# Performance work log

Hardware: AMD Instinct MI355X
Metric: run time of the kernel (lower is better)

The kernel has to match this reference:

```python
import jax, jax.numpy as jnp
import numpy as np

D_MODEL = 1024
N_HEADS = 16
D_K = D_MODEL // N_HEADS
THETA = 10000.0
BATCH = 2
SEQ = 2048


def apply_rope(x, positions):
    # x: [B, H, S, d_k], positions: [S] int
    half = D_K // 2
    inv_freq = 1.0 / (THETA ** (jnp.arange(half, dtype=jnp.float32) * 2.0 / D_K))  # [half]
    ang = positions.astype(jnp.float32)[:, None] * inv_freq[None, :]  # [S, half]
    cos = jnp.cos(ang)
    sin = jnp.sin(ang)
    xr = x.reshape(x.shape[:-1] + (half, 2))
    x1, x2 = xr[..., 0], xr[..., 1]
    o1 = x1 * cos - x2 * sin
    o2 = x1 * sin + x2 * cos
    return jnp.stack([o1, o2], axis=-1).reshape(x.shape)


def setup_inputs() -> dict:
    key = jax.random.key(0)
    ks = jax.random.split(key, 5)
    scale = 1.0 / np.sqrt(D_MODEL)
    return {
        "x": jax.random.normal(ks[0], (BATCH, SEQ, D_MODEL), jnp.float32),
        "token_positions": jnp.arange(SEQ, dtype=jnp.int32),
        "Wq": jax.random.normal(ks[1], (D_MODEL, D_MODEL), jnp.float32) * scale,
        "Wk": jax.random.normal(ks[2], (D_MODEL, D_MODEL), jnp.float32) * scale,
        "Wv": jax.random.normal(ks[3], (D_MODEL, D_MODEL), jnp.float32) * scale,
        "Wo": jax.random.normal(ks[4], (D_MODEL, D_MODEL), jnp.float32) * scale,
    }


def reference(x, token_positions, Wq, Wk, Wv, Wo):
    B, S, _ = x.shape
    # projections (Linear with weight [out, in], no bias): y = x @ W^T
    def split_heads(t):
        return t.reshape(B, S, N_HEADS, D_K).transpose(0, 2, 1, 3)  # [B,H,S,d_k]

    Q = split_heads(x @ Wq.T)
    K = split_heads(x @ Wk.T)
    V = split_heads(x @ Wv.T)

    Q = apply_rope(Q, token_positions)
    K = apply_rope(K, token_positions)

    scores = jnp.einsum("bhqd,bhkd->bhqk", Q, K) / np.sqrt(D_K)
    causal = jnp.tril(jnp.ones((S, S), dtype=bool))
    scores = jnp.where(causal, scores, -jnp.inf)
    attn = jax.nn.softmax(scores, axis=-1)
    out = jnp.einsum("bhqk,bhkd->bhqd", attn, V)  # [B,H,S,d_k]
    out = out.transpose(0, 2, 1, 3).reshape(B, S, D_MODEL)
    return out @ Wo.T
```

## Files before the change

### kernel.cpp

```cpp
#include <hip/hip_runtime.h>
#include <hip/hip_bf16.h>


typedef __bf16 bf16x8 __attribute__((ext_vector_type(8)));
typedef __bf16 bf16x4 __attribute__((ext_vector_type(4)));
typedef float f32x4 __attribute__((ext_vector_type(4)));
typedef unsigned short ushort8 __attribute__((ext_vector_type(8)));

#define BATCH 2
#define SEQ 2048
#define NH 16
#define DK 64
#define DM 1024
#define BH (BATCH*NH)
#define M_TOT (BATCH*SEQ)

__device__ __forceinline__ void gload16(const void* g, void* l) {
    __builtin_amdgcn_global_load_lds((const __attribute__((address_space(1))) void*)g,
                                     (__attribute__((address_space(3))) void*)l, 16, 0, 0);
}

__global__ void cvt_kernel(const float* __restrict__ s, __bf16* __restrict__ d, int n) {
    int i = (blockIdx.x * blockDim.x + threadIdx.x) * 4;
    if (i >= n) return;
    float4 v = *(const float4*)(s + i);
    bf16x4 o;
    o[0] = (__bf16)v.x; o[1] = (__bf16)v.y; o[2] = (__bf16)v.z; o[3] = (__bf16)v.w;
    *(bf16x4*)(d + i) = o;
}

__global__ void cvt4_kernel(const float* __restrict__ s0, const float* __restrict__ s1,
                            const float* __restrict__ s2, const float* __restrict__ s3,
                            __bf16* __restrict__ d0, __bf16* __restrict__ d1,
                            __bf16* __restrict__ d2, __bf16* __restrict__ d3, int n) {
    const int z = blockIdx.y;
    const float* s = (z == 0) ? s0 : (z == 1) ? s1 : (z == 2) ? s2 : s3;
    __bf16* d = (z == 0) ? d0 : (z == 1) ? d1 : (z == 2) ? d2 : d3;
    int i = (blockIdx.x * blockDim.x + threadIdx.x) * 4;
    if (i >= n) return;
    float4 v = *(const float4*)(s + i);
    bf16x4 o;
    o[0] = (__bf16)v.x; o[1] = (__bf16)v.y; o[2] = (__bf16)v.z; o[3] = (__bf16)v.w;
    *(bf16x4*)(d + i) = o;
}

__device__ __forceinline__ void gemm_tile_compute(
    const __bf16* __restrict__ A, const __bf16* __restrict__ W,
    int m0, int n0, int K, __bf16* sA, __bf16* sB, f32x4 (&acc)[4][4])
{
    const int t = threadIdx.x;
    const int lane = t & 63, wid = t >> 6;
    const int wr = wid >> 1, wc = wid & 1;
    const int g = lane >> 4, l15 = lane & 15;

    f32x4 zero = {0.f, 0.f, 0.f, 0.f};
#pragma unroll
    for (int mt = 0; mt < 4; ++mt)
#pragma unroll
        for (int nt = 0; nt < 4; ++nt) acc[mt][nt] = zero;

    for (int k0 = 0; k0 < K; k0 += 32) {
        __syncthreads();
#pragma unroll
        for (int rnd = 0; rnd < 2; ++rnd) {
            int s = rnd * 256 + t;
            int row = s >> 2, ch = s & 3;
            __bf16* dstA = sA + (rnd * 256 + wid * 64) * 8;
            __bf16* dstB = sB + (rnd * 256 + wid * 64) * 8;
            gload16(A + (size_t)(m0 + row) * K + k0 + ch * 8, dstA);
            gload16(W + (size_t)(n0 + row) * K + k0 + ch * 8, dstB);
        }
        __syncthreads();
        bf16x8 af[4], bfr[4];
#pragma unroll
        for (int mt = 0; mt < 4; ++mt)
            af[mt] = *(const bf16x8*)&sA[(wr * 64 + mt * 16 + l15) * 32 + g * 8];
#pragma unroll
        for (int nt = 0; nt < 4; ++nt)
            bfr[nt] = *(const bf16x8*)&sB[(wc * 64 + nt * 16 + l15) * 32 + g * 8];
#pragma unroll
        for (int mt = 0; mt < 4; ++mt)
#pragma unroll
            for (int nt = 0; nt < 4; ++nt)
                acc[mt][nt] = __builtin_amdgcn_mfma_f32_16x16x32_bf16(af[mt], bfr[nt], acc[mt][nt], 0, 0, 0);
    }
}

__global__ __launch_bounds__(256) void gemm_qkv(
    const __bf16* __restrict__ xb, const __bf16* __restrict__ wqkv,
    __bf16* __restrict__ Qb, __bf16* __restrict__ Kb, __bf16* __restrict__ VTb)
{
    __shared__ __align__(16) __bf16 sA[128 * 32], sB[128 * 32];
    int id = blockIdx.x + 24 * blockIdx.y;
    id = (id & 7) * 96 + (id >> 3);
    const int m0 = (id / 24) * 128, n0 = (id % 24) * 128;

    f32x4 acc[4][4];
    gemm_tile_compute(xb, wqkv, m0, n0, DM, sA, sB, acc);

    const int t = threadIdx.x, lane = t & 63, wid = t >> 6;
    const int wr = wid >> 1, wc = wid & 1, g = lane >> 4, l15 = lane & 15;
#pragma unroll
    for (int mt = 0; mt < 4; ++mt)
#pragma unroll
        for (int nt = 0; nt < 4; ++nt)
#pragma unroll
            for (int r = 0; r < 4; ++r) {
                int m = m0 + wr * 64 + mt * 16 + g * 4 + r;
                int n = n0 + wc * 64 + nt * 16 + l15;
                int z = n >> 10, hd = n & 1023, h = hd >> 6, d = hd & 63;
                int b = m >> 11, s = m & 2047;
                __bf16 v = (__bf16)acc[mt][nt][r];
                if (z == 0)
                    Qb[(((size_t)(b * NH + h)) * SEQ + s) * DK + d] = v;
                else if (z == 1)
                    Kb[(((size_t)(b * NH + h)) * SEQ + s) * DK + d] = v;
                else
                    VTb[(((size_t)(b * NH + h)) * DK + d) * SEQ + s] = v;
            }
}

__global__ __launch_bounds__(256) void gemm_out(
    const __bf16* __restrict__ AO, const __bf16* __restrict__ wo, float* __restrict__ out)
{
    __shared__ __align__(16) __bf16 sA[128 * 32], sB[128 * 32];
    int id = blockIdx.x + 8 * blockIdx.y;
    id = (id & 7) * 32 + (id >> 3);
    const int m0 = (id / 8) * 128, n0 = (id % 8) * 128;

    f32x4 acc[4][4];
    gemm_tile_compute(AO, wo, m0, n0, DM, sA, sB, acc);

    const int t = threadIdx.x, lane = t & 63, wid = t >> 6;
    const int wr = wid >> 1, wc = wid & 1, g = lane >> 4, l15 = lane & 15;
#pragma unroll
    for (int mt = 0; mt < 4; ++mt)
#pragma unroll
        for (int nt = 0; nt < 4; ++nt)
#pragma unroll
            for (int r = 0; r < 4; ++r) {
                int m = m0 + wr * 64 + mt * 16 + g * 4 + r;
                int n = n0 + wc * 64 + nt * 16 + l15;
                out[(size_t)m * DM + n] = acc[mt][nt][r];
            }
}

__global__ __launch_bounds__(256) void rope_kernel(
    __bf16* __restrict__ Qb, __bf16* __restrict__ Kb, const int* __restrict__ pos)
{
    __shared__ float ctab[32], stab[32];
    const int s = blockIdx.x;
    const int t = threadIdx.x;
    if (t < 32) {
        float invf = exp2f(-13.287712379549449f * (float)t * (1.0f / 32.0f));
        float ang = (float)pos[s] * invf;
        float sn, cs;
        sincosf(ang, &sn, &cs);
        ctab[t] = cs; stab[t] = sn;
    }
    __syncthreads();
#pragma unroll
    for (int u = 0; u < 8; ++u) {
        int id = u * 256 + t;
        int i = id & 31;
        int bh = (id >> 5) & 31;
        int isK = id >> 10;
        __bf16* P = isK ? Kb : Qb;
        float qs = isK ? 1.0f : 0.125f;
        __bf16* p = P + ((size_t)bh * SEQ + s) * DK + i * 2;
        float x1 = (float)p[0], x2 = (float)p[1];
        float c = ctab[i], sn = stab[i];
        p[0] = (__bf16)(qs * (x1 * c - x2 * sn));
        p[1] = (__bf16)(qs * (x1 * sn + x2 * c));
    }
}

__global__ __launch_bounds__(256, 2) void attn_kernel(
    const __bf16* __restrict__ Qb, const __bf16* __restrict__ Kb,
    const __bf16* __restrict__ VTb, __bf16* __restrict__ AO)
{
    __shared__ __align__(16) __bf16 sK[2][64 * 64];
    __shared__ __align__(16) __bf16 sV[2][64 * 64];
    __shared__ __align__(16) __bf16 sP[4 * 16 * 64];

    const int n = blockIdx.x;
    const int xcd = n & 7, slot = n >> 3;
    const int bh = xcd * 4 + (slot >> 4);
    const int x = slot & 15;
    const int t = threadIdx.x, lane = t & 63, wid = t >> 6;
    const int g = lane >> 4, l15 = lane & 15;

    const size_t baseQK = (size_t)bh * SEQ * DK;
    const size_t baseVT = (size_t)bh * DK * SEQ;
    const int b = bh >> 4, h = bh & 15;

    const char* Kt0 = (const char*)(Kb + baseQK);
    const char* Vt0 = (const char*)(VTb + baseVT);
    char* myP = (char*)sP + wid * 2048;
    f32x4 zero = {0.f, 0.f, 0.f, 0.f};

    auto stage_tile = [&](int kt, int bq) {
        const char* Kt = Kt0 + (size_t)kt * 64 * 128;
        const char* Vt = Vt0 + (size_t)kt * 128;
#pragma unroll
        for (int cc = 0; cc < 2; ++cc) {
            int c = t + cc * 256;
            int r = c >> 3, pp = c & 7;
            int p = pp ^ (r & 7);
            char* bK = (char*)sK[bq] + (cc * 256 + wid * 64) * 16;
            char* bV = (char*)sV[bq] + (cc * 256 + wid * 64) * 16;
            gload16(Kt + (size_t)r * 128 + p * 16, bK);
            gload16(Vt + (size_t)r * (SEQ * 2) + p * 16, bV);
        }
    };

    for (int ph = 0; ph < 2; ++ph) {
        const int j = ph ? (31 - x) : x;
        const int qrow_w = j * 64 + wid * 16;
        const int ktmax = j;

        bf16x8 qf[2];
        {
            const __bf16* qp = Qb + baseQK + (size_t)(qrow_w + l15) * DK;
            qf[0] = *(const bf16x8*)(qp + g * 8);
            qf[1] = *(const bf16x8*)(qp + 32 + g * 8);
        }

        f32x4 oacc[4];
        float mrow[4], lacc[4];
#pragma unroll
        for (int dt = 0; dt < 4; ++dt) oacc[dt] = zero;
#pragma unroll
        for (int r = 0; r < 4; ++r) { mrow[r] = -3e38f; lacc[r] = 0.f; }

        stage_tile(0, 0);
        __syncthreads();
        int cur = 0;

        for (int kt = 0; kt <= ktmax; ++kt) {
            if (kt < ktmax) stage_tile(kt + 1, cur ^ 1);

            f32x4 sacc[4];
#pragma unroll
            for (int nt = 0; nt < 4; ++nt) {
                sacc[nt] = zero;
                int row = nt * 16 + l15;
#pragma unroll
                for (int ks = 0; ks < 2; ++ks) {
                    bf16x8 kf = *(const bf16x8*)((const char*)sK[cur] + row * 128 +
                                                 ((ks * 64 + g * 16) ^ ((row & 7) << 4)));
                    sacc[nt] = __builtin_amdgcn_mfma_f32_16x16x32_bf16(qf[ks], kf, sacc[nt], 0, 0, 0);
                }
            }

            if (kt == ktmax) {
#pragma unroll
                for (int nt = 0; nt < 4; ++nt)
#pragma unroll
                    for (int r = 0; r < 4; ++r) {
                        int kv = kt * 64 + nt * 16 + l15;
                        int q = qrow_w + g * 4 + r;
                        if (kv > q) sacc[nt][r] = -3e38f;
                    }
            }

#pragma unroll
            for (int r = 0; r < 4; ++r) {
                float tm = fmaxf(fmaxf(sacc[0][r], sacc[1][r]), fmaxf(sacc[2][r], sacc[3][r]));
#pragma unroll
                for (int msk = 1; msk < 16; msk <<= 1) tm = fmaxf(tm, __shfl_xor(tm, msk));
                if (tm > mrow[r] + 8.0f) {
                    float sc = __expf(mrow[r] - tm);
                    mrow[r] = tm;
                    lacc[r] *= sc;
#pragma unroll
                    for (int dt = 0; dt < 4; ++dt) oacc[dt][r] *= sc;
                }
#pragma unroll
                for (int nt = 0; nt < 4; ++nt) {
                    float p = __expf(sacc[nt][r] - mrow[r]);
                    sacc[nt][r] = p;
                    lacc[r] += p;
                }
            }

#pragma unroll
            for (int nt = 0; nt < 4; ++nt)
#pragma unroll
                for (int r = 0; r < 4; ++r) {
                    int row = g * 4 + r;
                    *(__bf16*)(myP + row * 128 +
                               ((nt * 32 + l15 * 2) ^ ((row & 7) << 4))) = (__bf16)sacc[nt][r];
                }

#pragma unroll
            for (int ks = 0; ks < 2; ++ks) {
                bf16x8 pf = *(const bf16x8*)(myP + l15 * 128 +
                                             ((ks * 64 + g * 16) ^ ((l15 & 7) << 4)));
#pragma unroll
                for (int dt = 0; dt < 4; ++dt) {
                    int row = dt * 16 + l15;
                    bf16x8 vf = *(const bf16x8*)((const char*)sV[cur] + row * 128 +
                                                 ((ks * 64 + g * 16) ^ ((row & 7) << 4)));
                    oacc[dt] = __builtin_amdgcn_mfma_f32_16x16x32_bf16(pf, vf, oacc[dt], 0, 0, 0);
                }
            }

            __syncthreads();
            cur ^= 1;
        }

#pragma unroll
        for (int r = 0; r < 4; ++r) {
            float rs = lacc[r];
#pragma unroll
            for (int msk = 1; msk < 16; msk <<= 1) rs += __shfl_xor(rs, msk);
            float inv = 1.0f / rs;
            int srow = qrow_w + g * 4 + r;
            size_t obase = ((size_t)b * SEQ + srow) * DM + h * DK;
#pragma unroll
            for (int dt = 0; dt < 4; ++dt)
                AO[obase + dt * 16 + l15] = (__bf16)(oacc[dt][r] * inv);
        }
    }
}

extern "C" void kernel_launch(void* const* d_in, const int* in_sizes, int n_in,
                              void* d_out, int out_size, void* d_ws, size_t ws_size,
                              hipStream_t stream) {
    (void)in_sizes; (void)n_in; (void)out_size; (void)ws_size;
    const float* x  = (const float*)d_in[0];
    const int*  pos = (const int*)d_in[1];
    const float* Wq = (const float*)d_in[2];
    const float* Wk = (const float*)d_in[3];
    const float* Wv = (const float*)d_in[4];
    const float* Wo = (const float*)d_in[5];
    float* out = (float*)d_out;

    char* ws = (char*)d_ws;
    __bf16* xb   = (__bf16*)ws; ws += (size_t)M_TOT * DM * 2;
    __bf16* wqkv = (__bf16*)ws; ws += (size_t)3 * DM * DM * 2;
    __bf16* wob  = (__bf16*)ws; ws += (size_t)DM * DM * 2;
    __bf16* Qb   = (__bf16*)ws; ws += (size_t)BH * SEQ * DK * 2;
    __bf16* Kb   = (__bf16*)ws; ws += (size_t)BH * SEQ * DK * 2;
    __bf16* VTb  = (__bf16*)ws; ws += (size_t)BH * SEQ * DK * 2;
    __bf16* AOb  = (__bf16*)ws; ws += (size_t)M_TOT * DM * 2;

    const int nx = M_TOT * DM, nw = DM * DM;
    cvt_kernel<<<nx / 4 / 256, 256, 0, stream>>>(x, xb, nx);
    cvt4_kernel<<<dim3(nw / 4 / 256, 4), 256, 0, stream>>>(
        Wq, Wk, Wv, Wo, wqkv, wqkv + nw, wqkv + 2 * nw, wob, nw);

    gemm_qkv<<<dim3(24, M_TOT / 128), 256, 0, stream>>>(xb, wqkv, Qb, Kb, VTb);
    rope_kernel<<<SEQ, 256, 0, stream>>>(Qb, Kb, pos);
    attn_kernel<<<512, 256, 0, stream>>>(Qb, Kb, VTb, AOb);
    gemm_out<<<dim3(8, M_TOT / 128), 256, 0, stream>>>(AOb, wob, out);
}
```

Baseline: 220.3 us.

## Merge convert kernels, split attention into one query tile per block, use exp2

The two fp32-to-bf16 conversion kernels become a single launch. Attention blocks now each handle one 64-row query tile instead of a paired short/long tile, which doubles the grid to 1024 blocks and interleaves long and short tiles across blocks. Q is pre-scaled by log2(e) so the softmax can use exp2f, and MFMA sections are wrapped with s_setprio. Both GEMMs gain a launch_bounds occupancy hint. The risk is that per-block causal work becomes unbalanced, since pairing tiles no longer evens out the load inside a block.

```diff
diff --git a/kernel.cpp b/kernel.cpp
--- a/kernel.cpp
+++ b/kernel.cpp
@@ -14,34 +14,35 @@
 #define DM 1024
 #define BH (BATCH*NH)
 #define M_TOT (BATCH*SEQ)
+#define NX (M_TOT*DM)
+#define NW (DM*DM)
 
 __device__ __forceinline__ void gload16(const void* g, void* l) {
     __builtin_amdgcn_global_load_lds((const __attribute__((address_space(1))) void*)g,
                                      (__attribute__((address_space(3))) void*)l, 16, 0, 0);
 }
 
-__global__ void cvt_kernel(const float* __restrict__ s, __bf16* __restrict__ d, int n) {
-    int i = (blockIdx.x * blockDim.x + threadIdx.x) * 4;
-    if (i >= n) return;
-    float4 v = *(const float4*)(s + i);
+__global__ void cvt_all(const float* __restrict__ x,
+                        const float* __restrict__ Wq, const float* __restrict__ Wk,
+                        const float* __restrict__ Wv, const float* __restrict__ Wo,
+                        __bf16* __restrict__ xb, __bf16* __restrict__ wqkv,
+                        __bf16* __restrict__ wob) {
+    int i4 = (blockIdx.x * blockDim.x + threadIdx.x) * 4;
+    const float* s;
+    __bf16* d;
+    int off;
+    if (i4 < NX) { s = x; d = xb; off = i4; }
+    else {
+        int j = i4 - NX;
+        int z = j >> 20;
+        off = j & (NW - 1);
+        s = (z == 0) ? Wq : (z == 1) ? Wk : (z == 2) ? Wv : Wo;
+        d = (z == 3) ? wob : wqkv + (size_t)z * NW;
+    }
+    float4 v = *(const float4*)(s + off);
     bf16x4 o;
     o[0] = (__bf16)v.x; o[1] = (__bf16)v.y; o[2] = (__bf16)v.z; o[3] = (__bf16)v.w;
-    *(bf16x4*)(d + i) = o;
-}
-
-__global__ void cvt4_kernel(const float* __restrict__ s0, const float* __restrict__ s1,
-                            const float* __restrict__ s2, const float* __restrict__ s3,
-                            __bf16* __restrict__ d0, __bf16* __restrict__ d1,
-                            __bf16* __restrict__ d2, __bf16* __restrict__ d3, int n) {
-    const int z = blockIdx.y;
-    const float* s = (z == 0) ? s0 : (z == 1) ? s1 : (z == 2) ? s2 : s3;
-    __bf16* d = (z == 0) ? d0 : (z == 1) ? d1 : (z == 2) ? d2 : d3;
-    int i = (blockIdx.x * blockDim.x + threadIdx.x) * 4;
-    if (i >= n) return;
-    float4 v = *(const float4*)(s + i);
-    bf16x4 o;
-    o[0] = (__bf16)v.x; o[1] = (__bf16)v.y; o[2] = (__bf16)v.z; o[3] = (__bf16)v.w;
-    *(bf16x4*)(d + i) = o;
+    *(bf16x4*)(d + off) = o;
 }
 
 __device__ __forceinline__ void gemm_tile_compute(
@@ -86,7 +87,7 @@
     }
 }
 
-__global__ __launch_bounds__(256) void gemm_qkv(
+__global__ __launch_bounds__(256, 2) void gemm_qkv(
     const __bf16* __restrict__ xb, const __bf16* __restrict__ wqkv,
     __bf16* __restrict__ Qb, __bf16* __restrict__ Kb, __bf16* __restrict__ VTb)
 {
@@ -120,7 +121,7 @@
             }
 }
 
-__global__ __launch_bounds__(256) void gemm_out(
+__global__ __launch_bounds__(256, 2) void gemm_out(
     const __bf16* __restrict__ AO, const __bf16* __restrict__ wo, float* __restrict__ out)
 {
     __shared__ __align__(16) __bf16 sA[128 * 32], sB[128 * 32];
@@ -166,7 +167,7 @@
         int bh = (id >> 5) & 31;
         int isK = id >> 10;
         __bf16* P = isK ? Kb : Qb;
-        float qs = isK ? 1.0f : 0.125f;
+        float qs = isK ? 1.0f : (0.125f * 1.44269504088896f);
         __bf16* p = P + ((size_t)bh * SEQ + s) * DK + i * 2;
         float x1 = (float)p[0], x2 = (float)p[1];
         float c = ctab[i], sn = stab[i];
@@ -185,14 +186,17 @@
 
     const int n = blockIdx.x;
     const int xcd = n & 7, slot = n >> 3;
-    const int bh = xcd * 4 + (slot >> 4);
-    const int x = slot & 15;
+    const int bh = xcd * 4 + (slot >> 5);
+    const int js = slot & 31;
+    const int j = (js & 1) ? (js >> 1) : (31 - (js >> 1));
     const int t = threadIdx.x, lane = t & 63, wid = t >> 6;
     const int g = lane >> 4, l15 = lane & 15;
 
     const size_t baseQK = (size_t)bh * SEQ * DK;
     const size_t baseVT = (size_t)bh * DK * SEQ;
     const int b = bh >> 4, h = bh & 15;
+    const int qrow_w = j * 64 + wid * 16;
+    const int ktmax = j;
 
     const char* Kt0 = (const char*)(Kb + baseQK);
     const char* Vt0 = (const char*)(VTb + baseVT);
@@ -214,114 +218,113 @@
         }
     };
 
-    for (int ph = 0; ph < 2; ++ph) {
-        const int j = ph ? (31 - x) : x;
-        const int qrow_w = j * 64 + wid * 16;
-        const int ktmax = j;
-
-        bf16x8 qf[2];
-        {
-            const __bf16* qp = Qb + baseQK + (size_t)(qrow_w + l15) * DK;
-            qf[0] = *(const bf16x8*)(qp + g * 8);
-            qf[1] = *(const bf16x8*)(qp + 32 + g * 8);
-        }
-
-        f32x4 oacc[4];
-        float mrow[4], lacc[4];
-#pragma unroll
-        for (int dt = 0; dt < 4; ++dt) oacc[dt] = zero;
-#pragma unroll
-        for (int r = 0; r < 4; ++r) { mrow[r] = -3e38f; lacc[r] = 0.f; }
-
-        stage_tile(0, 0);
+    stage_tile(0, 0);
+
+    bf16x8 qf[2];
+    {
+        const __bf16* qp = Qb + baseQK + (size_t)(qrow_w + l15) * DK;
+        qf[0] = *(const bf16x8*)(qp + g * 8);
+        qf[1] = *(const bf16x8*)(qp + 32 + g * 8);
+    }
+
+    f32x4 oacc[4];
+    float mrow[4], lacc[4];
+#pragma unroll
+    for (int dt = 0; dt < 4; ++dt) oacc[dt] = zero;
+#pragma unroll
+    for (int r = 0; r < 4; ++r) { mrow[r] = -3e38f; lacc[r] = 0.f; }
+
+    __syncthreads();
+    int cur = 0;
+
+    for (int kt = 0; kt <= ktmax; ++kt) {
+        if (kt < ktmax) stage_tile(kt + 1, cur ^ 1);
+
+        f32x4 sacc[4];
+        __builtin_amdgcn_s_setprio(1);
+#pragma unroll
+        for (int nt = 0; nt < 4; ++nt) {
+            sacc[nt] = zero;
+            int row = nt * 16 + l15;
+#pragma unroll
+            for (int ks = 0; ks < 2; ++ks) {
+                bf16x8 kf = *(const bf16x8*)((const char*)sK[cur] + row * 128 +
+                                             ((ks * 64 + g * 16) ^ ((row & 7) << 4)));
+                sacc[nt] = __builtin_amdgcn_mfma_f32_16x16x32_bf16(qf[ks], kf, sacc[nt], 0, 0, 0);
+            }
+        }
+        __builtin_amdgcn_s_setprio(0);
+
+        if (kt == ktmax) {
+#pragma unroll
+            for (int nt = 0; nt < 4; ++nt)
+#pragma unroll
+                for (int r = 0; r < 4; ++r) {
+                    int kv = kt * 64 + nt * 16 + l15;
+                    int q = qrow_w + g * 4 + r;
+                    if (kv > q) sacc[nt][r] = -3e38f;
+                }
+        }
+
+#pragma unroll
+        for (int r = 0; r < 4; ++r) {
+            float tm = fmaxf(fmaxf(sacc[0][r], sacc[1][r]), fmaxf(sacc[2][r], sacc[3][r]));
+#pragma unroll
+            for (int msk = 1; msk < 16; msk <<= 1) tm = fmaxf(tm, __shfl_xor(tm, msk));
+            if (tm > mrow[r] + 11.5416f) {
+                float sc = exp2f(mrow[r] - tm);
+                mrow[r] = tm;
+                lacc[r] *= sc;
+#pragma unroll
+                for (int dt = 0; dt < 4; ++dt) oacc[dt][r] *= sc;
+            }
+#pragma unroll
+            for (int nt = 0; nt < 4; ++nt) {
+                float p = exp2f(sacc[nt][r] - mrow[r]);
+                sacc[nt][r] = p;
+                lacc[r] += p;
+            }
+        }
+
+#pragma unroll
+        for (int nt = 0; nt < 4; ++nt)
+#pragma unroll
+            for (int r = 0; r < 4; ++r) {
+                int row = g * 4 + r;
+                *(__bf16*)(myP + row * 128 +
+                           ((nt * 32 + l15 * 2) ^ ((row & 7) << 4))) = (__bf16)sacc[nt][r];
+            }
+
+        __builtin_amdgcn_s_setprio(1);
+#pragma unroll
+        for (int ks = 0; ks < 2; ++ks) {
+            bf16x8 pf = *(const bf16x8*)(myP + l15 * 128 +
+                                         ((ks * 64 + g * 16) ^ ((l15 & 7) << 4)));
+#pragma unroll
+            for (int dt = 0; dt < 4; ++dt) {
+                int row = dt * 16 + l15;
+                bf16x8 vf = *(const bf16x8*)((const char*)sV[cur] + row * 128 +
+                                             ((ks * 64 + g * 16) ^ ((row & 7) << 4)));
+                oacc[dt] = __builtin_amdgcn_mfma_f32_16x16x32_bf16(pf, vf, oacc[dt], 0, 0, 0);
+            }
+        }
+        __builtin_amdgcn_s_setprio(0);
+
         __syncthreads();
-        int cur = 0;
-
-        for (int kt = 0; kt <= ktmax; ++kt) {
-            if (kt < ktmax) stage_tile(kt + 1, cur ^ 1);
-
-            f32x4 sacc[4];
-#pragma unroll
-            for (int nt = 0; nt < 4; ++nt) {
-                sacc[nt] = zero;
-                int row = nt * 16 + l15;
-#pragma unroll
-                for (int ks = 0; ks < 2; ++ks) {
-                    bf16x8 kf = *(const bf16x8*)((const char*)sK[cur] + row * 128 +
-                                                 ((ks * 64 + g * 16) ^ ((row & 7) << 4)));
-                    sacc[nt] = __builtin_amdgcn_mfma_f32_16x16x32_bf16(qf[ks], kf, sacc[nt], 0, 0, 0);
-                }
-            }
-
-            if (kt == ktmax) {
-#pragma unroll
-                for (int nt = 0; nt < 4; ++nt)
-#pragma unroll
-                    for (int r = 0; r < 4; ++r) {
-                        int kv = kt * 64 + nt * 16 + l15;
-                        int q = qrow_w + g * 4 + r;
-                        if (kv > q) sacc[nt][r] = -3e38f;
-                    }
-            }
-
-#pragma unroll
-            for (int r = 0; r < 4; ++r) {
-                float tm = fmaxf(fmaxf(sacc[0][r], sacc[1][r]), fmaxf(sacc[2][r], sacc[3][r]));
-#pragma unroll
-                for (int msk = 1; msk < 16; msk <<= 1) tm = fmaxf(tm, __shfl_xor(tm, msk));
-                if (tm > mrow[r] + 8.0f) {
-                    float sc = __expf(mrow[r] - tm);
-                    mrow[r] = tm;
-                    lacc[r] *= sc;
-#pragma unroll
-                    for (int dt = 0; dt < 4; ++dt) oacc[dt][r] *= sc;
-                }
-#pragma unroll
-                for (int nt = 0; nt < 4; ++nt) {
-                    float p = __expf(sacc[nt][r] - mrow[r]);
-                    sacc[nt][r] = p;
-                    lacc[r] += p;
-                }
-            }
-
-#pragma unroll
-            for (int nt = 0; nt < 4; ++nt)
-#pragma unroll
-                for (int r = 0; r < 4; ++r) {
-                    int row = g * 4 + r;
-                    *(__bf16*)(myP + row * 128 +
-                               ((nt * 32 + l15 * 2) ^ ((row & 7) << 4))) = (__bf16)sacc[nt][r];
-                }
-
-#pragma unroll
-            for (int ks = 0; ks < 2; ++ks) {
-                bf16x8 pf = *(const bf16x8*)(myP + l15 * 128 +
-                                             ((ks * 64 + g * 16) ^ ((l15 & 7) << 4)));
-#pragma unroll
-                for (int dt = 0; dt < 4; ++dt) {
-                    int row = dt * 16 + l15;
-                    bf16x8 vf = *(const bf16x8*)((const char*)sV[cur] + row * 128 +
-                                                 ((ks * 64 + g * 16) ^ ((row & 7) << 4)));
-                    oacc[dt] = __builtin_amdgcn_mfma_f32_16x16x32_bf16(pf, vf, oacc[dt], 0, 0, 0);
-                }
-            }
-
-            __syncthreads();
-            cur ^= 1;
-        }
-
-#pragma unroll
-        for (int r = 0; r < 4; ++r) {
-            float rs = lacc[r];
-#pragma unroll
-            for (int msk = 1; msk < 16; msk <<= 1) rs += __shfl_xor(rs, msk);
-            float inv = 1.0f / rs;
-            int srow = qrow_w + g * 4 + r;
-            size_t obase = ((size_t)b * SEQ + srow) * DM + h * DK;
-#pragma unroll
-            for (int dt = 0; dt < 4; ++dt)
-                AO[obase + dt * 16 + l15] = (__bf16)(oacc[dt][r] * inv);
-        }
+        cur ^= 1;
+    }
+
+#pragma unroll
+    for (int r = 0; r < 4; ++r) {
+        float rs = lacc[r];
+#pragma unroll
+        for (int msk = 1; msk < 16; msk <<= 1) rs += __shfl_xor(rs, msk);
+        float inv = 1.0f / rs;
+        int srow = qrow_w + g * 4 + r;
+        size_t obase = ((size_t)b * SEQ + srow) * DM + h * DK;
+#pragma unroll
+        for (int dt = 0; dt < 4; ++dt)
+            AO[obase + dt * 16 + l15] = (__bf16)(oacc[dt][r] * inv);
     }
 }
 
@@ -346,13 +349,11 @@
     __bf16* VTb  = (__bf16*)ws; ws += (size_t)BH * SEQ * DK * 2;
     __bf16* AOb  = (__bf16*)ws; ws += (size_t)M_TOT * DM * 2;
 
-    const int nx = M_TOT * DM, nw = DM * DM;
-    cvt_kernel<<<nx / 4 / 256, 256, 0, stream>>>(x, xb, nx);
-    cvt4_kernel<<<dim3(nw / 4 / 256, 4), 256, 0, stream>>>(
-        Wq, Wk, Wv, Wo, wqkv, wqkv + nw, wqkv + 2 * nw, wob, nw);
+    const int ntot = NX + 4 * NW;
+    cvt_all<<<ntot / 4 / 256, 256, 0, stream>>>(x, Wq, Wk, Wv, Wo, xb, wqkv, wob);
 
     gemm_qkv<<<dim3(24, M_TOT / 128), 256, 0, stream>>>(xb, wqkv, Qb, Kb, VTb);
     rope_kernel<<<SEQ, 256, 0, stream>>>(Qb, Kb, pos);
-    attn_kernel<<<512, 256, 0, stream>>>(Qb, Kb, VTb, AOb);
+    attn_kernel<<<1024, 256, 0, stream>>>(Qb, Kb, VTb, AOb);
     gemm_out<<<dim3(8, M_TOT / 128), 256, 0, stream>>>(AOb, wob, out);
 }
```

After: 257.3 us. 16.8% more time.
